# Kernel tuning notes

Hardware: AMD Instinct MI355X
Metric: run time of the kernel (lower is better)

Reference implementation:

```python
import jax, jax.numpy as jnp
import numpy as np

NUM_HEAD = 8
EMBED_DIM = 512


def setup_inputs() -> dict:
    key = jax.random.key(0)
    ks = jax.random.split(key, 9)
    B, N, D = 4, 2048, 512
    # xavier_uniform bound for square [D, D] weights
    bound = float(np.sqrt(6.0 / (D + EMBED_DIM)))
    return {
        "q": jax.random.normal(ks[0], (B, N, D), jnp.float32),
        "k": jax.random.normal(ks[1], (B, N, D), jnp.float32),
        "v": jax.random.normal(ks[2], (B, N, D), jnp.float32),
        "Wq": jax.random.uniform(ks[3], (D, EMBED_DIM), jnp.float32, -bound, bound),
        "Wk": jax.random.uniform(ks[4], (D, EMBED_DIM), jnp.float32, -bound, bound),
        "Wv": jax.random.uniform(ks[5], (D, EMBED_DIM), jnp.float32, -bound, bound),
        "bq": jnp.zeros((EMBED_DIM,), jnp.float32),
        "bk": jnp.zeros((EMBED_DIM,), jnp.float32),
        "bv": jnp.zeros((EMBED_DIM,), jnp.float32),
    }


def reference(q, k, v, Wq, Wk, Wv, bq, bk, bv):
    h = NUM_HEAD
    ch = EMBED_DIM // h
    B, N, _ = q.shape
    # linear projections
    Q = q @ Wq + bq  # [B, N, E]
    K = k @ Wk + bk
    V = v @ Wv + bv
    # split heads: b n (h ch) -> b h n ch
    Q = Q.reshape(B, N, h, ch).transpose(0, 2, 1, 3)
    K = K.reshape(B, N, h, ch).transpose(0, 2, 1, 3)
    V = V.reshape(B, N, h, ch).transpose(0, 2, 1, 3)
    scale = 1.0 / np.sqrt(ch).astype(np.float32)
    scores = jnp.einsum("bhqc,bhkc->bhqk", Q, K) * scale  # [B, h, N, N]
    attn = jax.nn.softmax(scores, axis=-1)
    out = jnp.einsum("bhqk,bhkc->bhqc", attn, V)  # [B, h, N, ch]
    # merge heads: b h n ch -> b n (h ch)
    return out.transpose(0, 2, 1, 3).reshape(B, N, EMBED_DIM)
```

## Files before the change

### kernel.cpp

```cpp
#include <hip/hip_runtime.h>
#include <hip/hip_bf16.h>
#include <cstdint>

#define B_ 4
#define N_ 2048
#define D_ 512
#define E_ 512
#define H_ 8
#define CH_ 64
#define M_ (B_*N_)

typedef __attribute__((ext_vector_type(8))) short bf16x8;
typedef __attribute__((ext_vector_type(4))) float f32x4;
typedef __attribute__((ext_vector_type(16))) float f32x16;
using u16 = unsigned short;
using u32 = unsigned int;

__device__ __forceinline__ u16 f2bf(float f) {
  union { __hip_bfloat16 h; u16 u; } cv;
  cv.h = __float2bfloat16(f);
  return cv.u;
}

__device__ __forceinline__ float fexp2(float x) {
#if __has_builtin(__builtin_amdgcn_exp2f)
  return __builtin_amdgcn_exp2f(x);
#else
  return exp2f(x);
#endif
}

__device__ __forceinline__ void async16(const void* g, void* l) {
  __builtin_amdgcn_global_load_lds(
      (__attribute__((address_space(1))) void*)(g),
      (__attribute__((address_space(3))) void*)(l),
      16, 0, 0);
}

__global__ void prep(const float* __restrict__ q, const float* __restrict__ k,
                     const float* __restrict__ v,
                     const float* __restrict__ Wq, const float* __restrict__ Wk,
                     const float* __restrict__ Wv,
                     u16* __restrict__ qb, u16* __restrict__ kb, u16* __restrict__ vb,
                     u16* __restrict__ tq, u16* __restrict__ tk, u16* __restrict__ tv) {
  int bid = blockIdx.x;
  if (bid < 12288) {
    int t = bid >> 12;
    const float* in = (t == 0) ? q : (t == 1 ? k : v);
    u16* outp = (t == 0) ? qb : (t == 1 ? kb : vb);
    int i = ((bid & 4095) << 8) + threadIdx.x;
    float4 f = reinterpret_cast<const float4*>(in)[i];
    ushort4 o;
    o.x = f2bf(f.x); o.y = f2bf(f.y); o.z = f2bf(f.z); o.w = f2bf(f.w);
    reinterpret_cast<ushort4*>(outp)[i] = o;
  } else {
    bid -= 12288;
    int t = bid >> 10;
    const float* W = (t == 0) ? Wq : (t == 1 ? Wk : Wv);
    u16* T = (t == 0) ? tq : (t == 1 ? tk : tv);
    int idx = ((bid & 1023) << 8) + threadIdx.x;
    int e = idx >> 9, kd = idx & 511;
    T[idx] = f2bf(W[kd * E_ + e]);
  }
}

#define GBM 128
#define GBN 128
#define GBK 64

__global__ __launch_bounds__(256) void proj_gemm(
    const u16* __restrict__ xq, const u16* __restrict__ xk, const u16* __restrict__ xv,
    const u16* __restrict__ wtq, const u16* __restrict__ wtk, const u16* __restrict__ wtv,
    const float* __restrict__ bq, const float* __restrict__ bk, const float* __restrict__ bv,
    u16* __restrict__ Qp, u16* __restrict__ Kp, u16* __restrict__ Vp) {
  const int z = blockIdx.z;
  const u16* X  = (z == 0) ? xq : (z == 1 ? xk : xv);
  const u16* WT = (z == 0) ? wtq : (z == 1 ? wtk : wtv);
  const float* bias = (z == 0) ? bq : (z == 1 ? bk : bv);
  u16* Out = (z == 0) ? Qp : (z == 1 ? Kp : Vp);
  const float scale = (z == 0) ? 0.18033688011112042f : 1.0f;
  const bool vlayout = (z == 2);

  __shared__ __align__(16) u16 As[GBM * GBK];
  __shared__ __align__(16) u16 Bs[GBN * GBK];

  const int tid = threadIdx.x;
  const int l = tid & 63, w = tid >> 6;
  const int wr = w >> 1, wc = w & 1;
  const int m0 = blockIdx.y * GBM;
  const int e0 = blockIdx.x * GBN;

  f32x4 acc[4][4] = {};

  for (int ks = 0; ks < D_ / GBK; ++ks) {
    const int k0 = ks * GBK;
#pragma unroll
    for (int i = 0; i < 4; ++i) {
      int o = i * 4096 + tid * 16;
      int row = o >> 7, colb = o & 127;
      int scol = colb ^ ((row & 7) << 4);
      async16((const char*)X  + ((size_t)(m0 + row) * D_ + k0) * 2 + scol, (char*)As + o);
      async16((const char*)WT + ((size_t)(e0 + row) * D_ + k0) * 2 + scol, (char*)Bs + o);
    }
    __syncthreads();
#pragma unroll
    for (int kk = 0; kk < 2; ++kk) {
      bf16x8 af[4], bfr[4];
#pragma unroll
      for (int m = 0; m < 4; ++m) {
        int row = wr * 64 + m * 16 + (l & 15);
        int addr = (row << 7) + kk * 64 + ((l >> 4) << 4);
        addr ^= (row & 7) << 4;
        af[m] = *reinterpret_cast<const bf16x8*>((const char*)As + addr);
      }
#pragma unroll
      for (int n = 0; n < 4; ++n) {
        int row = wc * 64 + n * 16 + (l & 15);
        int addr = (row << 7) + kk * 64 + ((l >> 4) << 4);
        addr ^= (row & 7) << 4;
        bfr[n] = *reinterpret_cast<const bf16x8*>((const char*)Bs + addr);
      }
#pragma unroll
      for (int m = 0; m < 4; ++m)
#pragma unroll
        for (int n = 0; n < 4; ++n)
          acc[m][n] = __builtin_amdgcn_mfma_f32_16x16x32_bf16(af[m], bfr[n], acc[m][n], 0, 0, 0);
    }
    __syncthreads();
  }

#pragma unroll
  for (int m = 0; m < 4; ++m) {
#pragma unroll
    for (int n = 0; n < 4; ++n) {
      int ge = e0 + wc * 64 + n * 16 + (l & 15);
      int h = ge >> 6, c = ge & 63;
      float bv_ = bias[ge];
      int gm0 = m0 + wr * 64 + m * 16 + ((l >> 4) << 2);
      int b = gm0 >> 11, nn0 = gm0 & 2047;
      if (vlayout) {
        short4 sv;
#pragma unroll
        for (int j = 0; j < 4; ++j)
          ((u16*)&sv)[j] = f2bf((acc[m][n][j] + bv_) * scale);
        int np = (((nn0 >> 2) ^ (nn0 >> 3)) & 1) ? (nn0 ^ 12) : nn0;
        *reinterpret_cast<short4*>(
            &Out[(((size_t)b * H_ + h) * CH_ + c) * N_ + np]) = sv;
      } else {
#pragma unroll
        for (int j = 0; j < 4; ++j) {
          u16 oval = f2bf((acc[m][n][j] + bv_) * scale);
          Out[((((size_t)b * H_ + h) * N_ + nn0 + j) << 6) + c] = oval;
        }
      }
    }
  }
}

#define QBLK 128
#define KVB 64
#define NT (N_ / KVB)

#define MFMA32(A, Bv, C) __builtin_amdgcn_mfma_f32_32x32x16_bf16((A), (Bv), (C), 0, 0, 0)

__global__ __launch_bounds__(256, 2) void attn_kernel(
    const u16* __restrict__ Qp, const u16* __restrict__ Kp, const u16* __restrict__ Vp,
    float* __restrict__ out) {
  __shared__ __align__(16) u16 Kb[2][KVB * 64];
  __shared__ __align__(16) u16 Vb[2][64 * KVB];

  const int tid = threadIdx.x;
  const int l = tid & 63, w = tid >> 6;
  const int qcol = l & 31, hi = l >> 5;

  const int beta = blockIdx.x;
  const int xcd = beta & 7, kk_ = beta >> 3;
  const int bh = xcd * 4 + (kk_ >> 4);
  const int qt = kk_ & 15;

  const u16* Qh = Qp + (size_t)bh * N_ * CH_;
  const u16* Kh = Kp + (size_t)bh * N_ * CH_;
  const u16* Vh = Vp + (size_t)bh * CH_ * N_;
  const int bb = bh >> 3, hh = bh & 7;
  const int qrow = qt * QBLK + w * 32 + qcol;

  bf16x8 qf[4];
  {
    const u16* qptr = Qh + (size_t)qrow * CH_;
#pragma unroll
    for (int ks = 0; ks < 4; ++ks)
      qf[ks] = *reinterpret_cast<const bf16x8*>(qptr + ks * 16 + hi * 8);
  }

  f32x16 o0 = {}, o1 = {};
  float lrun = 0.f;

  const int rowA = qcol << 7;
  const int swz  = (l & 7) << 4;
  const int hi16 = hi << 4;

#define STAGE(BUF, KV) do {                                                      \
    _Pragma("unroll")                                                            \
    for (int i = 0; i < 2; ++i) {                                                \
      int o = i * 4096 + tid * 16;                                               \
      int row = o >> 7, colb = o & 127;                                          \
      int scol = colb ^ ((row & 7) << 4);                                        \
      async16((const char*)Kh + ((size_t)((KV) + row) << 7) + scol,              \
              (char*)&Kb[BUF][0] + o);                                           \
      async16((const char*)Vh + ((size_t)row * N_ + (KV)) * 2 + scol,            \
              (char*)&Vb[BUF][0] + o);                                           \
    } } while (0)

#define TILE(BUF, T) do {                                                        \
    if ((T) + 1 < NT) STAGE(BUF ^ 1, ((T) + 1) * KVB);                           \
    f32x16 s0 = {}, s1 = {};                                                     \
    __builtin_amdgcn_s_setprio(1);                                               \
    _Pragma("unroll")                                                            \
    for (int ks = 0; ks < 4; ++ks) {                                             \
      int col = (ks * 32 + hi16) ^ swz;                                          \
      bf16x8 k0 = *reinterpret_cast<const bf16x8*>((const char*)&Kb[BUF][0] + rowA + col);        \
      bf16x8 k1 = *reinterpret_cast<const bf16x8*>((const char*)&Kb[BUF][0] + 4096 + rowA + col); \
      s0 = MFMA32(k0, qf[ks], s0);                                               \
      s1 = MFMA32(k1, qf[ks], s1);                                               \
    }                                                                            \
    __builtin_amdgcn_s_setprio(0);                                               \
                  \
    _Pragma("unroll")                                                            \
    for (int r = 0; r < 16; ++r) { s0[r] = fexp2(s0[r]); s1[r] = fexp2(s1[r]); } \
    {                                                                            \
      float t0 = (s0[0] + s0[1]) + (s0[2] + s0[3]);                              \
      float t1 = (s0[4] + s0[5]) + (s0[6] + s0[7]);                              \
      float t2 = (s0[8] + s0[9]) + (s0[10] + s0[11]);                            \
      float t3 = (s0[12] + s0[13]) + (s0[14] + s0[15]);                          \
      float t4 = (s1[0] + s1[1]) + (s1[2] + s1[3]);                              \
      float t5 = (s1[4] + s1[5]) + (s1[6] + s1[7]);                              \
      float t6 = (s1[8] + s1[9]) + (s1[10] + s1[11]);                            \
      float t7 = (s1[12] + s1[13]) + (s1[14] + s1[15]);                          \
      float rsum = ((t0 + t1) + (t2 + t3)) + ((t4 + t5) + (t6 + t7));            \
      rsum += __shfl_xor(rsum, 32);                                              \
      lrun += rsum;                                                              \
    }                                                                            \
                  \
    __builtin_amdgcn_s_setprio(1);                                               \
    _Pragma("unroll")                                                            \
    for (int ks = 0; ks < 4; ++ks) {                                             \
      const f32x16& sv = (ks < 2) ? s0 : s1;                                     \
      const int b0 = 8 * (ks & 1);                                               \
      union { u16 us[8]; bf16x8 v8; } pu;                                        \
      _Pragma("unroll")                                                          \
      for (int j = 0; j < 8; ++j) pu.us[j] = f2bf(sv[b0 + j]);                   \
      int col = (ks * 32 + hi16) ^ swz;                                          \
      bf16x8 v0 = *reinterpret_cast<const bf16x8*>((const char*)&Vb[BUF][0] + rowA + col);        \
      bf16x8 v1 = *reinterpret_cast<const bf16x8*>((const char*)&Vb[BUF][0] + 4096 + rowA + col); \
      o0 = MFMA32(v0, pu.v8, o0);                                                \
      o1 = MFMA32(v1, pu.v8, o1);                                                \
    }                                                                            \
    __builtin_amdgcn_s_setprio(0);                                               \
    __syncthreads();                                                             \
  } while (0)

  STAGE(0, 0);
  __syncthreads();

  for (int tt = 0; tt < NT; tt += 2) {
    TILE(0, tt);
    TILE(1, tt + 1);
  }

  float inv = 1.0f / lrun;
  const size_t obase = ((size_t)bb * N_ + qrow) * E_ + hh * CH_;
#pragma unroll
  for (int m = 0; m < 2; ++m) {
    const f32x16& ov = m ? o1 : o0;
#pragma unroll
    for (int g4 = 0; g4 < 4; ++g4) {
      float4 st;
      st.x = ov[g4 * 4 + 0] * inv;
      st.y = ov[g4 * 4 + 1] * inv;
      st.z = ov[g4 * 4 + 2] * inv;
      st.w = ov[g4 * 4 + 3] * inv;
      *reinterpret_cast<float4*>(out + obase + m * 32 + g4 * 8 + hi * 4) = st;
    }
  }
#undef STAGE
#undef TILE
}

extern "C" void kernel_launch(void* const* d_in, const int* in_sizes, int n_in,
                              void* d_out, int out_size, void* d_ws, size_t ws_size,
                              hipStream_t stream) {
  const float* q  = (const float*)d_in[0];
  const float* k  = (const float*)d_in[1];
  const float* v  = (const float*)d_in[2];
  const float* Wq = (const float*)d_in[3];
  const float* Wk = (const float*)d_in[4];
  const float* Wv = (const float*)d_in[5];
  const float* bq = (const float*)d_in[6];
  const float* bk = (const float*)d_in[7];
  const float* bv = (const float*)d_in[8];
  float* out = (float*)d_out;

  u16* qb  = (u16*)d_ws;
  u16* kb  = qb + (size_t)M_ * D_;
  u16* vb  = kb + (size_t)M_ * D_;
  u16* wtq = vb + (size_t)M_ * D_;
  u16* wtk = wtq + (size_t)D_ * E_;
  u16* wtv = wtk + (size_t)D_ * E_;
  u16* Qp  = wtv + (size_t)D_ * E_;
  u16* Kp  = Qp + (size_t)M_ * E_;
  u16* Vp  = Kp + (size_t)M_ * E_;

  prep<<<15360, 256, 0, stream>>>(q, k, v, Wq, Wk, Wv, qb, kb, vb, wtq, wtk, wtv);
  proj_gemm<<<dim3(E_ / GBN, M_ / GBM, 3), 256, 0, stream>>>(
      qb, kb, vb, wtq, wtk, wtv, bq, bk, bv, Qp, Kp, Vp);
  attn_kernel<<<512, 256, 0, stream>>>(Qp, Kp, Vp, out);
}
```

Baseline: 87.41 us.

## Switch attention to 16x16x32 MFMA with 64-row query tiles and more blocks

Rewrites the attention kernel to use 16x16x32 bf16 MFMA instead of 32x32x16. Each wave now owns 16 query rows, the query tile shrinks to 64, and twice as many blocks are launched with a launch bound of 4 blocks per CU. The V permutation written by the projection kernel changes to match the new P fragment layout. The aim is more parallelism and occupancy across CUs and fewer registers per thread. In exchange, each loaded K/V tile is reused by fewer query rows, so LDS and global traffic rise.

```diff
diff --git a/kernel.cpp b/kernel.cpp
--- a/kernel.cpp
+++ b/kernel.cpp
@@ -12,7 +12,6 @@
 
 typedef __attribute__((ext_vector_type(8))) short bf16x8;
 typedef __attribute__((ext_vector_type(4))) float f32x4;
-typedef __attribute__((ext_vector_type(16))) float f32x16;
 using u16 = unsigned short;
 using u32 = unsigned int;
 
@@ -143,7 +142,7 @@
 #pragma unroll
         for (int j = 0; j < 4; ++j)
           ((u16*)&sv)[j] = f2bf((acc[m][n][j] + bv_) * scale);
-        int np = (((nn0 >> 2) ^ (nn0 >> 3)) & 1) ? (nn0 ^ 12) : nn0;
+        int np = (nn0 & ~31) | ((nn0 & 12) << 1) | ((nn0 & 16) >> 2);
         *reinterpret_cast<short4*>(
             &Out[(((size_t)b * H_ + h) * CH_ + c) * N_ + np]) = sv;
       } else {
@@ -157,13 +156,13 @@
   }
 }
 
-#define QBLK 128
+#define QBLK 64
 #define KVB 64
 #define NT (N_ / KVB)
 
-#define MFMA32(A, Bv, C) __builtin_amdgcn_mfma_f32_32x32x16_bf16((A), (Bv), (C), 0, 0, 0)
-
-__global__ __launch_bounds__(256, 2) void attn_kernel(
+#define MFMA16(A, Bv, C) __builtin_amdgcn_mfma_f32_16x16x32_bf16((A), (Bv), (C), 0, 0, 0)
+
+__global__ __launch_bounds__(256, 4) void attn_kernel(
     const u16* __restrict__ Qp, const u16* __restrict__ Kp, const u16* __restrict__ Vp,
     float* __restrict__ out) {
   __shared__ __align__(16) u16 Kb[2][KVB * 64];
@@ -171,33 +170,32 @@
 
   const int tid = threadIdx.x;
   const int l = tid & 63, w = tid >> 6;
-  const int qcol = l & 31, hi = l >> 5;
+  const int qr = l & 15, g = l >> 4;
 
   const int beta = blockIdx.x;
   const int xcd = beta & 7, kk_ = beta >> 3;
-  const int bh = xcd * 4 + (kk_ >> 4);
-  const int qt = kk_ & 15;
+  const int bh = xcd * 4 + (kk_ >> 5);
+  const int qt = kk_ & 31;
 
   const u16* Qh = Qp + (size_t)bh * N_ * CH_;
   const u16* Kh = Kp + (size_t)bh * N_ * CH_;
   const u16* Vh = Vp + (size_t)bh * CH_ * N_;
   const int bb = bh >> 3, hh = bh & 7;
-  const int qrow = qt * QBLK + w * 32 + qcol;
-
-  bf16x8 qf[4];
+  const int qrow = qt * QBLK + w * 16 + qr;
+
+  bf16x8 qf[2];
   {
     const u16* qptr = Qh + (size_t)qrow * CH_;
 #pragma unroll
-    for (int ks = 0; ks < 4; ++ks)
-      qf[ks] = *reinterpret_cast<const bf16x8*>(qptr + ks * 16 + hi * 8);
-  }
-
-  f32x16 o0 = {}, o1 = {};
+    for (int kk = 0; kk < 2; ++kk)
+      qf[kk] = *reinterpret_cast<const bf16x8*>(qptr + kk * 32 + g * 8);
+  }
+
+  f32x4 oacc[4] = {};
   float lrun = 0.f;
 
-  const int rowA = qcol << 7;
-  const int swz  = (l & 7) << 4;
-  const int hi16 = hi << 4;
+  const int g16 = g << 4;
+  const int swz = (l & 7) << 4;
 
 #define STAGE(BUF, KV) do {                                                      \
     _Pragma("unroll")                                                            \
@@ -213,47 +211,49 @@
 
 #define TILE(BUF, T) do {                                                        \
     if ((T) + 1 < NT) STAGE(BUF ^ 1, ((T) + 1) * KVB);                           \
-    f32x16 s0 = {}, s1 = {};                                                     \
+    f32x4 sacc[4] = {};                                                          \
     __builtin_amdgcn_s_setprio(1);                                               \
     _Pragma("unroll")                                                            \
-    for (int ks = 0; ks < 4; ++ks) {                                             \
-      int col = (ks * 32 + hi16) ^ swz;                                          \
-      bf16x8 k0 = *reinterpret_cast<const bf16x8*>((const char*)&Kb[BUF][0] + rowA + col);        \
-      bf16x8 k1 = *reinterpret_cast<const bf16x8*>((const char*)&Kb[BUF][0] + 4096 + rowA + col); \
-      s0 = MFMA32(k0, qf[ks], s0);                                               \
-      s1 = MFMA32(k1, qf[ks], s1);                                               \
+    for (int kk = 0; kk < 2; ++kk) {                                             \
+      _Pragma("unroll")                                                          \
+      for (int n = 0; n < 4; ++n) {                                              \
+        int row = n * 16 + qr;                                                   \
+        int addr = ((row << 7) + kk * 64 + g16) ^ swz;                           \
+        bf16x8 kf = *reinterpret_cast<const bf16x8*>((const char*)&Kb[BUF][0] + addr); \
+        sacc[n] = MFMA16(kf, qf[kk], sacc[n]);                                   \
+      }                                                                          \
     }                                                                            \
     __builtin_amdgcn_s_setprio(0);                                               \
                   \
     _Pragma("unroll")                                                            \
-    for (int r = 0; r < 16; ++r) { s0[r] = fexp2(s0[r]); s1[r] = fexp2(s1[r]); } \
+    for (int n = 0; n < 4; ++n) {                                                \
+      sacc[n][0] = fexp2(sacc[n][0]); sacc[n][1] = fexp2(sacc[n][1]);            \
+      sacc[n][2] = fexp2(sacc[n][2]); sacc[n][3] = fexp2(sacc[n][3]);            \
+    }                                                                            \
     {                                                                            \
-      float t0 = (s0[0] + s0[1]) + (s0[2] + s0[3]);                              \
-      float t1 = (s0[4] + s0[5]) + (s0[6] + s0[7]);                              \
-      float t2 = (s0[8] + s0[9]) + (s0[10] + s0[11]);                            \
-      float t3 = (s0[12] + s0[13]) + (s0[14] + s0[15]);                          \
-      float t4 = (s1[0] + s1[1]) + (s1[2] + s1[3]);                              \
-      float t5 = (s1[4] + s1[5]) + (s1[6] + s1[7]);                              \
-      float t6 = (s1[8] + s1[9]) + (s1[10] + s1[11]);                            \
-      float t7 = (s1[12] + s1[13]) + (s1[14] + s1[15]);                          \
-      float rsum = ((t0 + t1) + (t2 + t3)) + ((t4 + t5) + (t6 + t7));            \
+      float t0 = (sacc[0][0] + sacc[0][1]) + (sacc[0][2] + sacc[0][3]);          \
+      float t1 = (sacc[1][0] + sacc[1][1]) + (sacc[1][2] + sacc[1][3]);          \
+      float t2 = (sacc[2][0] + sacc[2][1]) + (sacc[2][2] + sacc[2][3]);          \
+      float t3 = (sacc[3][0] + sacc[3][1]) + (sacc[3][2] + sacc[3][3]);          \
+      float rsum = (t0 + t1) + (t2 + t3);                                        \
+      rsum += __shfl_xor(rsum, 16);                                              \
       rsum += __shfl_xor(rsum, 32);                                              \
       lrun += rsum;                                                              \
     }                                                                            \
-                  \
+                 \
     __builtin_amdgcn_s_setprio(1);                                               \
     _Pragma("unroll")                                                            \
-    for (int ks = 0; ks < 4; ++ks) {                                             \
-      const f32x16& sv = (ks < 2) ? s0 : s1;                                     \
-      const int b0 = 8 * (ks & 1);                                               \
+    for (int kk = 0; kk < 2; ++kk) {                                             \
       union { u16 us[8]; bf16x8 v8; } pu;                                        \
       _Pragma("unroll")                                                          \
-      for (int j = 0; j < 8; ++j) pu.us[j] = f2bf(sv[b0 + j]);                   \
-      int col = (ks * 32 + hi16) ^ swz;                                          \
-      bf16x8 v0 = *reinterpret_cast<const bf16x8*>((const char*)&Vb[BUF][0] + rowA + col);        \
-      bf16x8 v1 = *reinterpret_cast<const bf16x8*>((const char*)&Vb[BUF][0] + 4096 + rowA + col); \
-      o0 = MFMA32(v0, pu.v8, o0);                                                \
-      o1 = MFMA32(v1, pu.v8, o1);                                                \
+      for (int j = 0; j < 8; ++j) pu.us[j] = f2bf(sacc[kk * 2 + (j >> 2)][j & 3]); \
+      _Pragma("unroll")                                                          \
+      for (int n = 0; n < 4; ++n) {                                              \
+        int row = n * 16 + qr;                                                   \
+        int addr = ((row << 7) + kk * 64 + g16) ^ swz;                           \
+        bf16x8 vf = *reinterpret_cast<const bf16x8*>((const char*)&Vb[BUF][0] + addr); \
+        oacc[n] = MFMA16(vf, pu.v8, oacc[n]);                                    \
+      }                                                                          \
     }                                                                            \
     __builtin_amdgcn_s_setprio(0);                                               \
     __syncthreads();                                                             \
@@ -270,17 +270,13 @@
   float inv = 1.0f / lrun;
   const size_t obase = ((size_t)bb * N_ + qrow) * E_ + hh * CH_;
 #pragma unroll
-  for (int m = 0; m < 2; ++m) {
-    const f32x16& ov = m ? o1 : o0;
-#pragma unroll
-    for (int g4 = 0; g4 < 4; ++g4) {
-      float4 st;
-      st.x = ov[g4 * 4 + 0] * inv;
-      st.y = ov[g4 * 4 + 1] * inv;
-      st.z = ov[g4 * 4 + 2] * inv;
-      st.w = ov[g4 * 4 + 3] * inv;
-      *reinterpret_cast<float4*>(out + obase + m * 32 + g4 * 8 + hi * 4) = st;
-    }
+  for (int n = 0; n < 4; ++n) {
+    float4 st;
+    st.x = oacc[n][0] * inv;
+    st.y = oacc[n][1] * inv;
+    st.z = oacc[n][2] * inv;
+    st.w = oacc[n][3] * inv;
+    *reinterpret_cast<float4*>(out + obase + n * 16 + g * 4) = st;
   }
 #undef STAGE
 #undef TILE
@@ -313,5 +309,5 @@
   prep<<<15360, 256, 0, stream>>>(q, k, v, Wq, Wk, Wv, qb, kb, vb, wtq, wtk, wtv);
   proj_gemm<<<dim3(E_ / GBN, M_ / GBM, 3), 256, 0, stream>>>(
       qb, kb, vb, wtq, wtk, wtv, bq, bk, bv, Qp, Kp, Vp);
-  attn_kernel<<<512, 256, 0, stream>>>(Qp, Kp, Vp, out);
-}
+  attn_kernel<<<1024, 256, 0, stream>>>(Qp, Kp, Vp, out);
+}
```

After: 91.45 us. 4.6% more time.

## Deepen attention K/V pipeline to four LDS buffers with prefetch distance two

Applied to the files above, without the earlier changes.

The attention kernel moves from double-buffered to quad-buffered K/V staging in shared memory. Loads are issued two tiles ahead, and each tile now waits with an explicit vmcnt(4) plus a raw s_barrier, replacing the full __syncthreads after every tile. The goal is to hide more global-load latency and cut barrier stalls. The cost is double the LDS footprint (64KB per block), which may lower occupancy below the two blocks per CU the launch bounds ask for, and the hand-counted vmcnt has to match the number of outstanding async copies.

```diff
diff --git a/kernel.cpp b/kernel.cpp
--- a/kernel.cpp
+++ b/kernel.cpp
@@ -166,8 +166,8 @@
 __global__ __launch_bounds__(256, 2) void attn_kernel(
     const u16* __restrict__ Qp, const u16* __restrict__ Kp, const u16* __restrict__ Vp,
     float* __restrict__ out) {
-  __shared__ __align__(16) u16 Kb[2][KVB * 64];
-  __shared__ __align__(16) u16 Vb[2][64 * KVB];
+  __shared__ __align__(16) u16 Kb[4][KVB * 64];
+  __shared__ __align__(16) u16 Vb[4][64 * KVB];
 
   const int tid = threadIdx.x;
   const int l = tid & 63, w = tid >> 6;
@@ -198,6 +198,12 @@
   const int rowA = qcol << 7;
   const int swz  = (l & 7) << 4;
   const int hi16 = hi << 4;
+
+#define VMCNT4 asm volatile("s_waitcnt vmcnt(4)" ::: "memory")
+#define VMCNT0 asm volatile("s_waitcnt vmcnt(0)" ::: "memory")
+#define RBAR   do { asm volatile("" ::: "memory");                               \
+                    __builtin_amdgcn_s_barrier();                                \
+                    asm volatile("" ::: "memory"); } while (0)
 
 #define STAGE(BUF, KV) do {                                                      \
     _Pragma("unroll")                                                            \
@@ -211,8 +217,7 @@
               (char*)&Vb[BUF][0] + o);                                           \
     } } while (0)
 
-#define TILE(BUF, T) do {                                                        \
-    if ((T) + 1 < NT) STAGE(BUF ^ 1, ((T) + 1) * KVB);                           \
+#define COMPUTE(BUF) do {                                                        \
     f32x16 s0 = {}, s1 = {};                                                     \
     __builtin_amdgcn_s_setprio(1);                                               \
     _Pragma("unroll")                                                            \
@@ -256,16 +261,26 @@
       o1 = MFMA32(v1, pu.v8, o1);                                                \
     }                                                                            \
     __builtin_amdgcn_s_setprio(0);                                               \
-    __syncthreads();                                                             \
   } while (0)
 
+#define TILE_S(BUF, T) do { VMCNT4; RBAR;                                        \
+    STAGE(((BUF) + 2) & 3, ((T) + 2) * KVB); COMPUTE(BUF); } while (0)
+#define TILE_N(BUF) do { VMCNT4; RBAR; COMPUTE(BUF); } while (0)
+#define TILE_L(BUF) do { VMCNT0; RBAR; COMPUTE(BUF); } while (0)
+
   STAGE(0, 0);
-  __syncthreads();
-
-  for (int tt = 0; tt < NT; tt += 2) {
-    TILE(0, tt);
-    TILE(1, tt + 1);
-  }
+  STAGE(1, KVB);
+
+  for (int tt = 0; tt < NT - 4; tt += 4) {
+    TILE_S(0, tt);
+    TILE_S(1, tt + 1);
+    TILE_S(2, tt + 2);
+    TILE_S(3, tt + 3);
+  }
+  TILE_S(0, NT - 4);
+  TILE_S(1, NT - 3);
+  TILE_N(2);
+  TILE_L(3);
 
   float inv = 1.0f / lrun;
   const size_t obase = ((size_t)bb * N_ + qrow) * E_ + hh * CH_;
@@ -283,7 +298,10 @@
     }
   }
 #undef STAGE
-#undef TILE
+#undef COMPUTE
+#undef TILE_S
+#undef TILE_N
+#undef TILE_L
 }
 
 extern "C" void kernel_launch(void* const* d_in, const int* in_sizes, int n_in,
```

Measured after the change: 87.41 us. About the same (-0.0%).

## Fuse input bf16 conversion into projection GEMM and split attention KV range

Applied to the files above, without the earlier changes.

The separate fp32-to-bf16 conversion pass over q/k/v is removed. The projection GEMM now loads fp32 activations straight into shared memory and converts them to bf16 when building MFMA fragments. Attention is split into two halves over the key/value sequence (split-K), doubling the grid to 1024 blocks and raising the occupancy hint to 4 blocks per CU. A new combine kernel sums the two partial outputs and divides by the summed row sums. The split adds fp32 partial-output traffic and an extra launch, and the GEMM's shared-memory A tile doubles in size, which may limit its occupancy.

```diff
diff --git a/kernel.cpp b/kernel.cpp
--- a/kernel.cpp
+++ b/kernel.cpp
@@ -37,51 +37,36 @@
       16, 0, 0);
 }
 
-__global__ void prep(const float* __restrict__ q, const float* __restrict__ k,
-                     const float* __restrict__ v,
-                     const float* __restrict__ Wq, const float* __restrict__ Wk,
-                     const float* __restrict__ Wv,
-                     u16* __restrict__ qb, u16* __restrict__ kb, u16* __restrict__ vb,
-                     u16* __restrict__ tq, u16* __restrict__ tk, u16* __restrict__ tv) {
+__global__ void prep_w(const float* __restrict__ Wq, const float* __restrict__ Wk,
+                       const float* __restrict__ Wv,
+                       u16* __restrict__ tq, u16* __restrict__ tk, u16* __restrict__ tv) {
   int bid = blockIdx.x;
-  if (bid < 12288) {
-    int t = bid >> 12;
-    const float* in = (t == 0) ? q : (t == 1 ? k : v);
-    u16* outp = (t == 0) ? qb : (t == 1 ? kb : vb);
-    int i = ((bid & 4095) << 8) + threadIdx.x;
-    float4 f = reinterpret_cast<const float4*>(in)[i];
-    ushort4 o;
-    o.x = f2bf(f.x); o.y = f2bf(f.y); o.z = f2bf(f.z); o.w = f2bf(f.w);
-    reinterpret_cast<ushort4*>(outp)[i] = o;
-  } else {
-    bid -= 12288;
-    int t = bid >> 10;
-    const float* W = (t == 0) ? Wq : (t == 1 ? Wk : Wv);
-    u16* T = (t == 0) ? tq : (t == 1 ? tk : tv);
-    int idx = ((bid & 1023) << 8) + threadIdx.x;
-    int e = idx >> 9, kd = idx & 511;
-    T[idx] = f2bf(W[kd * E_ + e]);
-  }
+  int t = bid >> 10;
+  const float* W = (t == 0) ? Wq : (t == 1 ? Wk : Wv);
+  u16* T = (t == 0) ? tq : (t == 1 ? tk : tv);
+  int idx = ((bid & 1023) << 8) + threadIdx.x;
+  int e = idx >> 9, kd = idx & 511;
+  T[idx] = f2bf(W[kd * E_ + e]);
 }
 
 #define GBM 128
 #define GBN 128
 #define GBK 64
 
-__global__ __launch_bounds__(256) void proj_gemm(
-    const u16* __restrict__ xq, const u16* __restrict__ xk, const u16* __restrict__ xv,
+__global__ __launch_bounds__(256, 3) void proj_gemm(
+    const float* __restrict__ xq, const float* __restrict__ xk, const float* __restrict__ xv,
     const u16* __restrict__ wtq, const u16* __restrict__ wtk, const u16* __restrict__ wtv,
     const float* __restrict__ bq, const float* __restrict__ bk, const float* __restrict__ bv,
     u16* __restrict__ Qp, u16* __restrict__ Kp, u16* __restrict__ Vp) {
   const int z = blockIdx.z;
-  const u16* X  = (z == 0) ? xq : (z == 1 ? xk : xv);
-  const u16* WT = (z == 0) ? wtq : (z == 1 ? wtk : wtv);
+  const float* X = (z == 0) ? xq : (z == 1 ? xk : xv);
+  const u16* WT  = (z == 0) ? wtq : (z == 1 ? wtk : wtv);
   const float* bias = (z == 0) ? bq : (z == 1 ? bk : bv);
   u16* Out = (z == 0) ? Qp : (z == 1 ? Kp : Vp);
   const float scale = (z == 0) ? 0.18033688011112042f : 1.0f;
   const bool vlayout = (z == 2);
 
-  __shared__ __align__(16) u16 As[GBM * GBK];
+  __shared__ __align__(16) float Asf[GBM * GBK];
   __shared__ __align__(16) u16 Bs[GBN * GBK];
 
   const int tid = threadIdx.x;
@@ -95,11 +80,17 @@
   for (int ks = 0; ks < D_ / GBK; ++ks) {
     const int k0 = ks * GBK;
 #pragma unroll
+    for (int i = 0; i < 8; ++i) {
+      int o = i * 4096 + tid * 16;
+      int row = o >> 8, colb = o & 255;
+      int scol = colb ^ ((row & 7) << 5);
+      async16((const char*)X + ((size_t)(m0 + row) * D_ + k0) * 4 + scol, (char*)Asf + o);
+    }
+#pragma unroll
     for (int i = 0; i < 4; ++i) {
       int o = i * 4096 + tid * 16;
       int row = o >> 7, colb = o & 127;
       int scol = colb ^ ((row & 7) << 4);
-      async16((const char*)X  + ((size_t)(m0 + row) * D_ + k0) * 2 + scol, (char*)As + o);
       async16((const char*)WT + ((size_t)(e0 + row) * D_ + k0) * 2 + scol, (char*)Bs + o);
     }
     __syncthreads();
@@ -109,9 +100,16 @@
 #pragma unroll
       for (int m = 0; m < 4; ++m) {
         int row = wr * 64 + m * 16 + (l & 15);
-        int addr = (row << 7) + kk * 64 + ((l >> 4) << 4);
-        addr ^= (row & 7) << 4;
-        af[m] = *reinterpret_cast<const bf16x8*>((const char*)As + addr);
+        int base = (row << 8) + kk * 128 + ((l >> 4) << 5);
+        int a0 = base ^ ((row & 7) << 5);
+        float4 fa = *reinterpret_cast<const float4*>((const char*)Asf + a0);
+        float4 fb = *reinterpret_cast<const float4*>((const char*)Asf + a0 + 16);
+        union { u16 us[8]; bf16x8 v8; } cu;
+        cu.us[0] = f2bf(fa.x); cu.us[1] = f2bf(fa.y);
+        cu.us[2] = f2bf(fa.z); cu.us[3] = f2bf(fa.w);
+        cu.us[4] = f2bf(fb.x); cu.us[5] = f2bf(fb.y);
+        cu.us[6] = f2bf(fb.z); cu.us[7] = f2bf(fb.w);
+        af[m] = cu.v8;
       }
 #pragma unroll
       for (int n = 0; n < 4; ++n) {
@@ -159,13 +157,13 @@
 
 #define QBLK 128
 #define KVB 64
-#define NT (N_ / KVB)
+#define NTH 16
 
 #define MFMA32(A, Bv, C) __builtin_amdgcn_mfma_f32_32x32x16_bf16((A), (Bv), (C), 0, 0, 0)
 
-__global__ __launch_bounds__(256, 2) void attn_kernel(
+__global__ __launch_bounds__(256, 4) void attn_kernel(
     const u16* __restrict__ Qp, const u16* __restrict__ Kp, const u16* __restrict__ Vp,
-    float* __restrict__ out) {
+    float* __restrict__ Op0, float* __restrict__ Op1, float* __restrict__ lp) {
   __shared__ __align__(16) u16 Kb[2][KVB * 64];
   __shared__ __align__(16) u16 Vb[2][64 * KVB];
 
@@ -174,9 +172,12 @@
   const int qcol = l & 31, hi = l >> 5;
 
   const int beta = blockIdx.x;
-  const int xcd = beta & 7, kk_ = beta >> 3;
-  const int bh = xcd * 4 + (kk_ >> 4);
-  const int qt = kk_ & 15;
+  const int xcd = beta & 7, r = beta >> 3;
+  const int bh = xcd * 4 + (r >> 5);
+  const int rem = r & 31;
+  const int qt = rem >> 1;
+  const int hf = rem & 1;
+  const int tb = hf * NTH;
 
   const u16* Qh = Qp + (size_t)bh * N_ * CH_;
   const u16* Kh = Kp + (size_t)bh * N_ * CH_;
@@ -211,8 +212,8 @@
               (char*)&Vb[BUF][0] + o);                                           \
     } } while (0)
 
-#define TILE(BUF, T) do {                                                        \
-    if ((T) + 1 < NT) STAGE(BUF ^ 1, ((T) + 1) * KVB);                           \
+#define TILE(BUF, TL) do {                                                       \
+    if ((TL) + 1 < NTH) STAGE((BUF) ^ 1, (tb + (TL) + 1) * KVB);                 \
     f32x16 s0 = {}, s1 = {};                                                     \
     __builtin_amdgcn_s_setprio(1);                                               \
     _Pragma("unroll")                                                            \
@@ -224,9 +225,8 @@
       s1 = MFMA32(k1, qf[ks], s1);                                               \
     }                                                                            \
     __builtin_amdgcn_s_setprio(0);                                               \
-                  \
     _Pragma("unroll")                                                            \
-    for (int r = 0; r < 16; ++r) { s0[r] = fexp2(s0[r]); s1[r] = fexp2(s1[r]); } \
+    for (int rr = 0; rr < 16; ++rr) { s0[rr] = fexp2(s0[rr]); s1[rr] = fexp2(s1[rr]); } \
     {                                                                            \
       float t0 = (s0[0] + s0[1]) + (s0[2] + s0[3]);                              \
       float t1 = (s0[4] + s0[5]) + (s0[6] + s0[7]);                              \
@@ -240,7 +240,6 @@
       rsum += __shfl_xor(rsum, 32);                                              \
       lrun += rsum;                                                              \
     }                                                                            \
-                  \
     __builtin_amdgcn_s_setprio(1);                                               \
     _Pragma("unroll")                                                            \
     for (int ks = 0; ks < 4; ++ks) {                                             \
@@ -259,15 +258,15 @@
     __syncthreads();                                                             \
   } while (0)
 
-  STAGE(0, 0);
+  STAGE(0, tb * KVB);
   __syncthreads();
 
-  for (int tt = 0; tt < NT; tt += 2) {
-    TILE(0, tt);
-    TILE(1, tt + 1);
-  }
-
-  float inv = 1.0f / lrun;
+  for (int tl = 0; tl < NTH; tl += 2) {
+    TILE(0, tl);
+    TILE(1, tl + 1);
+  }
+
+  float* Op = hf ? Op1 : Op0;
   const size_t obase = ((size_t)bb * N_ + qrow) * E_ + hh * CH_;
 #pragma unroll
   for (int m = 0; m < 2; ++m) {
@@ -275,15 +274,38 @@
 #pragma unroll
     for (int g4 = 0; g4 < 4; ++g4) {
       float4 st;
-      st.x = ov[g4 * 4 + 0] * inv;
-      st.y = ov[g4 * 4 + 1] * inv;
-      st.z = ov[g4 * 4 + 2] * inv;
-      st.w = ov[g4 * 4 + 3] * inv;
-      *reinterpret_cast<float4*>(out + obase + m * 32 + g4 * 8 + hi * 4) = st;
-    }
-  }
+      st.x = ov[g4 * 4 + 0];
+      st.y = ov[g4 * 4 + 1];
+      st.z = ov[g4 * 4 + 2];
+      st.w = ov[g4 * 4 + 3];
+      *reinterpret_cast<float4*>(Op + obase + m * 32 + g4 * 8 + hi * 4) = st;
+    }
+  }
+  if (hi == 0)
+    lp[hf * (32 * 2048) + bh * 2048 + qrow] = lrun;
 #undef STAGE
 #undef TILE
+}
+
+__global__ void combine(const float* __restrict__ Op0, const float* __restrict__ Op1,
+                        const float* __restrict__ lp, float* __restrict__ out) {
+  size_t i = (size_t)blockIdx.x * 256 + threadIdx.x;
+  size_t ef = i << 2;
+  int b = (int)(ef >> 20);
+  int n = (int)((ef >> 9) & 2047);
+  int h = (int)((ef & 511) >> 6);
+  int bh = b * H_ + h;
+  float l0 = lp[bh * 2048 + n];
+  float l1 = lp[32 * 2048 + bh * 2048 + n];
+  float inv = 1.0f / (l0 + l1);
+  float4 a = reinterpret_cast<const float4*>(Op0)[i];
+  float4 c = reinterpret_cast<const float4*>(Op1)[i];
+  float4 o;
+  o.x = (a.x + c.x) * inv;
+  o.y = (a.y + c.y) * inv;
+  o.z = (a.z + c.z) * inv;
+  o.w = (a.w + c.w) * inv;
+  reinterpret_cast<float4*>(out)[i] = o;
 }
 
 extern "C" void kernel_launch(void* const* d_in, const int* in_sizes, int n_in,
@@ -300,18 +322,19 @@
   const float* bv = (const float*)d_in[8];
   float* out = (float*)d_out;
 
-  u16* qb  = (u16*)d_ws;
-  u16* kb  = qb + (size_t)M_ * D_;
-  u16* vb  = kb + (size_t)M_ * D_;
-  u16* wtq = vb + (size_t)M_ * D_;
+  u16* wtq = (u16*)d_ws;
   u16* wtk = wtq + (size_t)D_ * E_;
   u16* wtv = wtk + (size_t)D_ * E_;
   u16* Qp  = wtv + (size_t)D_ * E_;
   u16* Kp  = Qp + (size_t)M_ * E_;
   u16* Vp  = Kp + (size_t)M_ * E_;
-
-  prep<<<15360, 256, 0, stream>>>(q, k, v, Wq, Wk, Wv, qb, kb, vb, wtq, wtk, wtv);
+  float* Op0 = (float*)(Vp + (size_t)M_ * E_);
+  float* Op1 = Op0 + (size_t)M_ * E_;
+  float* lp  = Op1 + (size_t)M_ * E_;
+
+  prep_w<<<3072, 256, 0, stream>>>(Wq, Wk, Wv, wtq, wtk, wtv);
   proj_gemm<<<dim3(E_ / GBN, M_ / GBM, 3), 256, 0, stream>>>(
-      qb, kb, vb, wtq, wtk, wtv, bq, bk, bv, Qp, Kp, Vp);
-  attn_kernel<<<512, 256, 0, stream>>>(Qp, Kp, Vp, out);
-}
+      q, k, v, wtq, wtk, wtv, bq, bk, bv, Qp, Kp, Vp);
+  attn_kernel<<<1024, 256, 0, stream>>>(Qp, Kp, Vp, Op0, Op1, lp);
+  combine<<<M_ * E_ / 4 / 256, 256, 0, stream>>>(Op0, Op1, lp, out);
+}
```

New measurement: 101.7 us. +16.4%, slower.
